# Kernel optimization log

Hardware: AMD Instinct MI355X
Metric: run time of the kernel (lower is better)

Reference implementation:

```python
import jax, jax.numpy as jnp
import numpy as np

# --- vocab metadata (replaces string itos_vocab lookups with precomputed tables) ---
# ids [0,128)   : pitch    'p0'..'p127'  (type 0)
# ids [128,289) : duration 'd0'..'d160'  (type 1)
# ids [289,390) : time     't0'..'t100'  (type 2)
# ids [390,518) : velocity 'v0'..'v127'  (type 3)
_tt = np.concatenate([np.full(128, 0), np.full(161, 1), np.full(101, 2), np.full(128, 3)]).astype(np.int32)
_tv = np.concatenate([np.arange(128), np.arange(161), np.arange(101), np.arange(128)]).astype(np.float32)
TOKEN_TYPE = jnp.asarray(_tt)   # [V]
TOKEN_VALUE = jnp.asarray(_tv)  # [V]
COEF = (1.0, 0.5, 0.5, 0.5, 0.5)  # matches init coeff_
# per-type numeric-distance normalizers (pitch unused: its branch is constant)
DENOM = jnp.array([1.0, 160.0, 100.0, 128.0], dtype=jnp.float32)
CW = jnp.array([COEF[1], COEF[2], COEF[3], COEF[4]], dtype=jnp.float32)

B, V, S = 32, 518, 2048


def setup_inputs() -> dict:
    key = jax.random.key(0)
    k1, k2 = jax.random.split(key)
    output = jax.random.normal(k1, (B, V, S), dtype=jnp.float32)  # logits [B, vocab, S]
    target = jax.random.randint(k2, (B, S), 0, V, dtype=jnp.int64)
    return {"output": output, "target": target}


def reference(output, target):
    target = target.astype(jnp.int32)
    # CrossEntropyLoss over class dim 1, mean over B*S
    lsm = jax.nn.log_softmax(output, axis=1)                       # [B,V,S]
    nll = -jnp.take_along_axis(lsm, target[:, None, :], axis=1)    # [B,1,S]
    loss = nll.mean()
    # faithful to source: softmax over last (sequence) dim, then argmax over vocab dim
    pred = jnp.argmax(jax.nn.softmax(output, axis=-1), axis=1)     # [B,S]
    pt, tt = TOKEN_TYPE[pred], TOKEN_TYPE[target]
    pv, tv = TOKEN_VALUE[pred], TOKEN_VALUE[target]
    diff = jnp.abs(pv - tv)
    # pitch branch: source compares 'pXX' != 'XX' which is always True -> constant coef[1]
    same_type = jnp.where(pt == 0, COEF[1], CW[pt] * diff / DENOM[pt])
    mask = jnp.where(pt != tt, COEF[0], same_type)                 # [B,S]
    high_cost = (loss * mask).mean()
    return loss + high_cost
```

## Files before the change

kernel.cpp:

```cpp
#include <hip/hip_runtime.h>

#define BV 518
#define SS 2048
#define NB 32

__device__ inline void tok_meta(int id, int& ty, float& val) {
    int base;
    if (id < 128)      { ty = 0; base = 0; }
    else if (id < 289) { ty = 1; base = 128; }
    else if (id < 390) { ty = 2; base = 289; }
    else               { ty = 3; base = 390; }
    val = (float)(id - base);
}

__global__ __launch_bounds__(256) void row_lse_kernel(const float* __restrict__ logits,
                                                      float* __restrict__ lse_row) {
    const int row = blockIdx.x;
    const float4* base4 = (const float4*)(logits + (size_t)row * SS);
    const int t = threadIdx.x;
    float4 x0 = base4[t];
    float4 x1 = base4[t + 256];
    float s = __expf(x0.x) + __expf(x0.y) + __expf(x0.z) + __expf(x0.w)
            + __expf(x1.x) + __expf(x1.y) + __expf(x1.z) + __expf(x1.w);
    #pragma unroll
    for (int off = 32; off; off >>= 1) s += __shfl_down(s, off);
    __shared__ float ws[4];
    if ((t & 63) == 0) ws[t >> 6] = s;
    __syncthreads();
    if (t == 0) lse_row[row] = __logf(ws[0] + ws[1] + ws[2] + ws[3]);
}

__global__ __launch_bounds__(256) void col_pass_kernel(const float* __restrict__ logits,
                                                       const int* __restrict__ target,
                                                       const float* __restrict__ lse_row,
                                                       float* __restrict__ acc) {
    const int b    = blockIdx.x >> 5;
    const int tile = blockIdx.x & 31;
    const int t    = threadIdx.x;
    const int sl   = t & 63;
    const int part = t >> 6;
    const int s    = tile * 64 + sl;

    __shared__ float slse[BV];
    for (int i = t; i < BV; i += 256) slse[i] = lse_row[b * BV + i];
    __syncthreads();

    const float* colbase = logits + (size_t)b * BV * SS + s;

    float sumexp = 0.f;
    float bscore = -1e30f;
    int   bidx   = 0x7fffffff;
    for (int v = part; v < BV; v += 4) {
        float x = colbase[(size_t)v * SS];
        sumexp += __expf(x);
        float sc = x - slse[v];
        if (sc > bscore) { bscore = sc; bidx = v; }
    }

    __shared__ float sse[4][64];
    __shared__ float sbs[4][64];
    __shared__ int   sbi[4][64];
    sse[part][sl] = sumexp;
    sbs[part][sl] = bscore;
    sbi[part][sl] = bidx;
    __syncthreads();

    if (t < 64) {
        float tot = 0.f, bs = -1e30f;
        int   bi  = 0x7fffffff;
        #pragma unroll
        for (int p = 0; p < 4; ++p) {
            tot += sse[p][t];
            float s2 = sbs[p][t]; int i2 = sbi[p][t];
            if (s2 > bs || (s2 == bs && i2 < bi)) { bs = s2; bi = i2; }
        }
        const int tgt = target[b * SS + t + tile * 64];
        const float ot = logits[(size_t)b * BV * SS + (size_t)tgt * SS + t + tile * 64];
        float nll = __logf(tot) - ot;

        int pt_, tt_; float pv_, tv_;
        tok_meta(bi, pt_, pv_);
        tok_meta(tgt, tt_, tv_);
        float mask;
        if (pt_ != tt_) {
            mask = 1.0f;
        } else if (pt_ == 0) {
            mask = 0.5f;
        } else {
            float dn = (pt_ == 1) ? 160.f : ((pt_ == 2) ? 100.f : 128.f);
            mask = 0.5f * fabsf(pv_ - tv_) / dn;
        }

        #pragma unroll
        for (int off = 32; off; off >>= 1) {
            nll  += __shfl_down(nll, off);
            mask += __shfl_down(mask, off);
        }
        if (t == 0) {
            atomicAdd(&acc[0], nll);
            atomicAdd(&acc[1], mask);
        }
    }
}

__global__ void finalize_kernel(const float* __restrict__ acc, float* __restrict__ out) {
    const float invN = 1.0f / (float)(NB * SS);
    float loss = acc[0] * invN;
    float mm   = acc[1] * invN;
    out[0] = loss * (1.0f + mm);
}

extern "C" void kernel_launch(void* const* d_in, const int* in_sizes, int n_in,
                              void* d_out, int out_size, void* d_ws, size_t ws_size,
                              hipStream_t stream) {
    const float* logits = (const float*)d_in[0];
    const int*   target = (const int*)d_in[1];
    float* outp = (float*)d_out;

    float* acc     = (float*)d_ws;
    float* lse_row = (float*)d_ws + 16;

    hipMemsetAsync(d_ws, 0, 64, stream);
    row_lse_kernel<<<NB * BV, 256, 0, stream>>>(logits, lse_row);
    col_pass_kernel<<<NB * (SS / 64), 256, 0, stream>>>(logits, target, lse_row, acc);
    finalize_kernel<<<1, 1, 0, stream>>>(acc, outp);
}
```

Measured before the change: 257.7 us.

## Split column pass over vocab halves with float4 loads and separate combine kernel

The column pass now uses float4 loads so each thread handles four sequence positions. Vocab is split into two halves across blocks, and partial sum-exp and argmax results are written to workspace. A new combine kernel merges the halves, computes the NLL and mask, and does one atomic per block instead of one per 64 columns. This aims to raise memory-level parallelism and coalescing in the column sweep, at the cost of an extra kernel launch and some partial-buffer traffic. Tie-breaking across the halves keeps the lower index only when scores are equal.

```diff
diff --git a/kernel.cpp b/kernel.cpp
--- a/kernel.cpp
+++ b/kernel.cpp
@@ -3,6 +3,7 @@
 #define BV 518
 #define SS 2048
 #define NB 32
+#define NCOL (NB * SS)
 
 __device__ inline void tok_meta(int id, int& ty, float& val) {
     int base;
@@ -30,76 +31,116 @@
     if (t == 0) lse_row[row] = __logf(ws[0] + ws[1] + ws[2] + ws[3]);
 }
 
-__global__ __launch_bounds__(256) void col_pass_kernel(const float* __restrict__ logits,
-                                                       const int* __restrict__ target,
-                                                       const float* __restrict__ lse_row,
-                                                       float* __restrict__ acc) {
-    const int b    = blockIdx.x >> 5;
-    const int tile = blockIdx.x & 31;
-    const int t    = threadIdx.x;
-    const int sl   = t & 63;
-    const int part = t >> 6;
-    const int s    = tile * 64 + sl;
+__global__ __launch_bounds__(256) void col_partial_kernel(const float* __restrict__ logits,
+                                                          const float* __restrict__ lse_row,
+                                                          float* __restrict__ pse,
+                                                          float* __restrict__ pbs,
+                                                          int*   __restrict__ pbi) {
+    const int bid   = blockIdx.x;
+    const int vh    = bid >> 8;
+    const int b     = (bid >> 3) & 31;
+    const int stile = bid & 7;
+    const int t     = threadIdx.x;
+    const int lane  = t & 63;
+    const int part  = t >> 6;
 
     __shared__ float slse[BV];
     for (int i = t; i < BV; i += 256) slse[i] = lse_row[b * BV + i];
     __syncthreads();
 
-    const float* colbase = logits + (size_t)b * BV * SS + s;
+    const int fidx = stile * 64 + lane;
+    const float4* rowbase = (const float4*)(logits + (size_t)b * BV * SS);
 
-    float sumexp = 0.f;
-    float bscore = -1e30f;
-    int   bidx   = 0x7fffffff;
-    for (int v = part; v < BV; v += 4) {
-        float x = colbase[(size_t)v * SS];
-        sumexp += __expf(x);
-        float sc = x - slse[v];
-        if (sc > bscore) { bscore = sc; bidx = v; }
+    const int vbase = vh ? 259 : 0;
+    const int vend  = vh ? BV  : 259;
+
+    float4 se = make_float4(0.f, 0.f, 0.f, 0.f);
+    float4 bs = make_float4(-1e30f, -1e30f, -1e30f, -1e30f);
+    int bix = 0x7fffffff, biy = 0x7fffffff, biz = 0x7fffffff, biw = 0x7fffffff;
+
+    #pragma unroll 4
+    for (int v = vbase + part; v < vend; v += 4) {
+        float4 x = rowbase[(size_t)v * (SS / 4) + fidx];
+        float l = slse[v];
+        se.x += __expf(x.x); se.y += __expf(x.y);
+        se.z += __expf(x.z); se.w += __expf(x.w);
+        float c0 = x.x - l, c1 = x.y - l, c2 = x.z - l, c3 = x.w - l;
+        if (c0 > bs.x) { bs.x = c0; bix = v; }
+        if (c1 > bs.y) { bs.y = c1; biy = v; }
+        if (c2 > bs.z) { bs.z = c2; biz = v; }
+        if (c3 > bs.w) { bs.w = c3; biw = v; }
     }
 
-    __shared__ float sse[4][64];
-    __shared__ float sbs[4][64];
-    __shared__ int   sbi[4][64];
-    sse[part][sl] = sumexp;
-    sbs[part][sl] = bscore;
-    sbi[part][sl] = bidx;
+    __shared__ float cse[4][256];
+    __shared__ float cbs[4][256];
+    __shared__ int   cbi[4][256];
+    const int sb = lane * 4;
+    cse[part][sb]     = se.x;  cse[part][sb + 1] = se.y;
+    cse[part][sb + 2] = se.z;  cse[part][sb + 3] = se.w;
+    cbs[part][sb]     = bs.x;  cbs[part][sb + 1] = bs.y;
+    cbs[part][sb + 2] = bs.z;  cbs[part][sb + 3] = bs.w;
+    cbi[part][sb]     = bix;   cbi[part][sb + 1] = biy;
+    cbi[part][sb + 2] = biz;   cbi[part][sb + 3] = biw;
     __syncthreads();
 
-    if (t < 64) {
-        float tot = 0.f, bs = -1e30f;
-        int   bi  = 0x7fffffff;
-        #pragma unroll
-        for (int p = 0; p < 4; ++p) {
-            tot += sse[p][t];
-            float s2 = sbs[p][t]; int i2 = sbi[p][t];
-            if (s2 > bs || (s2 == bs && i2 < bi)) { bs = s2; bi = i2; }
-        }
-        const int tgt = target[b * SS + t + tile * 64];
-        const float ot = logits[(size_t)b * BV * SS + (size_t)tgt * SS + t + tile * 64];
-        float nll = __logf(tot) - ot;
+    float tot = 0.f, best = -1e30f;
+    int   bi  = 0x7fffffff;
+    #pragma unroll
+    for (int p = 0; p < 4; ++p) {
+        tot += cse[p][t];
+        float s2 = cbs[p][t]; int i2 = cbi[p][t];
+        if (s2 > best || (s2 == best && i2 < bi)) { best = s2; bi = i2; }
+    }
+    const int g = (b * 8 + stile) * 256 + t;
+    pse[vh * NCOL + g] = tot;
+    pbs[vh * NCOL + g] = best;
+    pbi[vh * NCOL + g] = bi;
+}
 
-        int pt_, tt_; float pv_, tv_;
-        tok_meta(bi, pt_, pv_);
-        tok_meta(tgt, tt_, tv_);
-        float mask;
-        if (pt_ != tt_) {
-            mask = 1.0f;
-        } else if (pt_ == 0) {
-            mask = 0.5f;
-        } else {
-            float dn = (pt_ == 1) ? 160.f : ((pt_ == 2) ? 100.f : 128.f);
-            mask = 0.5f * fabsf(pv_ - tv_) / dn;
-        }
+__global__ __launch_bounds__(256) void combine_kernel(const float* __restrict__ logits,
+                                                      const int* __restrict__ target,
+                                                      const float* __restrict__ pse,
+                                                      const float* __restrict__ pbs,
+                                                      const int* __restrict__ pbi,
+                                                      float* __restrict__ acc) {
+    const int t = threadIdx.x;
+    const int g = blockIdx.x * 256 + t;
+    const int b = g >> 11;
+    const int s = g & 2047;
 
-        #pragma unroll
-        for (int off = 32; off; off >>= 1) {
-            nll  += __shfl_down(nll, off);
-            mask += __shfl_down(mask, off);
-        }
-        if (t == 0) {
-            atomicAdd(&acc[0], nll);
-            atomicAdd(&acc[1], mask);
-        }
+    float tot = pse[g] + pse[NCOL + g];
+    float b0 = pbs[g];        int i0 = pbi[g];
+    float b1 = pbs[NCOL + g]; int i1 = pbi[NCOL + g];
+    int bi = (b1 > b0) ? i1 : i0;
+
+    const int tgt = target[g];
+    const float ot = logits[(size_t)(b * BV + tgt) * SS + s];
+    float nll = __logf(tot) - ot;
+
+    int pt_, tt_; float pv_, tv_;
+    tok_meta(bi, pt_, pv_);
+    tok_meta(tgt, tt_, tv_);
+    float mask;
+    if (pt_ != tt_) {
+        mask = 1.0f;
+    } else if (pt_ == 0) {
+        mask = 0.5f;
+    } else {
+        float dn = (pt_ == 1) ? 160.f : ((pt_ == 2) ? 100.f : 128.f);
+        mask = 0.5f * fabsf(pv_ - tv_) / dn;
+    }
+
+    #pragma unroll
+    for (int off = 32; off; off >>= 1) {
+        nll  += __shfl_down(nll, off);
+        mask += __shfl_down(mask, off);
+    }
+    __shared__ float wn[4], wm[4];
+    if ((t & 63) == 0) { wn[t >> 6] = nll; wm[t >> 6] = mask; }
+    __syncthreads();
+    if (t == 0) {
+        atomicAdd(&acc[0], wn[0] + wn[1] + wn[2] + wn[3]);
+        atomicAdd(&acc[1], wm[0] + wm[1] + wm[2] + wm[3]);
     }
 }
 
@@ -118,10 +159,14 @@
     float* outp = (float*)d_out;
 
     float* acc     = (float*)d_ws;
-    float* lse_row = (float*)d_ws + 16;
+    float* lse_row = (float*)d_ws + 64;
+    float* pse     = (float*)d_ws + 17024;
+    float* pbs     = pse + 2 * NCOL;
+    int*   pbi     = (int*)(pbs + 2 * NCOL);
 
     hipMemsetAsync(d_ws, 0, 64, stream);
     row_lse_kernel<<<NB * BV, 256, 0, stream>>>(logits, lse_row);
-    col_pass_kernel<<<NB * (SS / 64), 256, 0, stream>>>(logits, target, lse_row, acc);
+    col_partial_kernel<<<512, 256, 0, stream>>>(logits, lse_row, pse, pbs, pbi);
+    combine_kernel<<<NCOL / 256, 256, 0, stream>>>(logits, target, pse, pbs, pbi, acc);
     finalize_kernel<<<1, 1, 0, stream>>>(acc, outp);
 }
```

Result: faster. 223.5 us (-13.3%).

## Fuse row LSE and column pass into one chunked kernel with atomic merge

Applied to the files above, without the earlier changes.

Replaces the separate row log-sum-exp pass and the full-column pass with one kernel. Each block handles a 16-row vocab chunk for one batch. It computes each row's LSE, then rereads those rows (likely from cache) to update per-column sumexp and argmax. Partial results go to global arrays through float atomicAdd and a packed 64-bit atomicMax, so the logits are effectively streamed from HBM once instead of twice. The cost is a large workspace memset, many global atomics, and an extra combine kernel.

```diff
diff --git a/kernel.cpp b/kernel.cpp
--- a/kernel.cpp
+++ b/kernel.cpp
@@ -3,6 +3,9 @@
 #define BV 518
 #define SS 2048
 #define NB 32
+#define NCOL (NB * SS)
+#define CHUNK 16
+#define NCH 33
 
 __device__ inline void tok_meta(int id, int& ty, float& val) {
     int base;
@@ -13,101 +16,135 @@
     val = (float)(id - base);
 }
 
-__global__ __launch_bounds__(256) void row_lse_kernel(const float* __restrict__ logits,
-                                                      float* __restrict__ lse_row) {
-    const int row = blockIdx.x;
-    const float4* base4 = (const float4*)(logits + (size_t)row * SS);
+__global__ __launch_bounds__(256, 2) void colfused_kernel(const float* __restrict__ logits,
+                                                          float* __restrict__ sacc,
+                                                          unsigned long long* __restrict__ pmax) {
+    const int bid = blockIdx.x;
+    const int b   = bid / NCH;
+    const int c   = bid % NCH;
+    const int v0  = c * CHUNK;
+    const int nrows = (BV - v0 < CHUNK) ? (BV - v0) : CHUNK;
     const int t = threadIdx.x;
-    float4 x0 = base4[t];
-    float4 x1 = base4[t + 256];
-    float s = __expf(x0.x) + __expf(x0.y) + __expf(x0.z) + __expf(x0.w)
-            + __expf(x1.x) + __expf(x1.y) + __expf(x1.z) + __expf(x1.w);
+    const int w = t >> 6;
+    const int l = t & 63;
+
+    __shared__ float slse[2][4];
+    const float* base = logits + (size_t)(b * BV) * SS;
+
+    float se[8];  float bsc[8];  int bvi[8];
     #pragma unroll
-    for (int off = 32; off; off >>= 1) s += __shfl_down(s, off);
-    __shared__ float ws[4];
-    if ((t & 63) == 0) ws[t >> 6] = s;
-    __syncthreads();
-    if (t == 0) lse_row[row] = __logf(ws[0] + ws[1] + ws[2] + ws[3]);
-}
+    for (int u = 0; u < 8; ++u) { se[u] = 0.f; bsc[u] = -1e30f; bvi[u] = 0; }
 
-__global__ __launch_bounds__(256) void col_pass_kernel(const float* __restrict__ logits,
-                                                       const int* __restrict__ target,
-                                                       const float* __restrict__ lse_row,
-                                                       float* __restrict__ acc) {
-    const int b    = blockIdx.x >> 5;
-    const int tile = blockIdx.x & 31;
-    const int t    = threadIdx.x;
-    const int sl   = t & 63;
-    const int part = t >> 6;
-    const int s    = tile * 64 + sl;
+    const int nsub = (nrows + 3) >> 2;
+    for (int sub = 0; sub < nsub; ++sub) {
+        const int r0 = sub * 4;
+        const int myrow = r0 + w;
+        if (myrow < nrows) {
+            const float4* rb = (const float4*)(base + (size_t)(v0 + myrow) * SS);
+            float s = 0.f;
+            #pragma unroll
+            for (int j = 0; j < 8; ++j) {
+                float4 x = rb[l + 64 * j];
+                s += __expf(x.x) + __expf(x.y) + __expf(x.z) + __expf(x.w);
+            }
+            #pragma unroll
+            for (int off = 32; off; off >>= 1) s += __shfl_xor(s, off);
+            if (l == 0) slse[sub & 1][w] = __logf(s);
+        }
+        __syncthreads();
 
-    __shared__ float slse[BV];
-    for (int i = t; i < BV; i += 256) slse[i] = lse_row[b * BV + i];
-    __syncthreads();
-
-    const float* colbase = logits + (size_t)b * BV * SS + s;
-
-    float sumexp = 0.f;
-    float bscore = -1e30f;
-    int   bidx   = 0x7fffffff;
-    for (int v = part; v < BV; v += 4) {
-        float x = colbase[(size_t)v * SS];
-        sumexp += __expf(x);
-        float sc = x - slse[v];
-        if (sc > bscore) { bscore = sc; bidx = v; }
+        const int rend = (nrows - r0 < 4) ? (nrows - r0) : 4;
+        for (int r = 0; r < rend; ++r) {
+            const int v = v0 + r0 + r;
+            const float lse = slse[sub & 1][r];
+            const float* rowp = base + (size_t)v * SS;
+            #pragma unroll
+            for (int u = 0; u < 8; ++u) {
+                float x = rowp[u * 256 + t];
+                se[u] += __expf(x);
+                float sc = x - lse;
+                if (sc > bsc[u]) { bsc[u] = sc; bvi[u] = v; }
+            }
+        }
     }
 
-    __shared__ float sse[4][64];
-    __shared__ float sbs[4][64];
-    __shared__ int   sbi[4][64];
-    sse[part][sl] = sumexp;
-    sbs[part][sl] = bscore;
-    sbi[part][sl] = bidx;
-    __syncthreads();
-
-    if (t < 64) {
-        float tot = 0.f, bs = -1e30f;
-        int   bi  = 0x7fffffff;
-        #pragma unroll
-        for (int p = 0; p < 4; ++p) {
-            tot += sse[p][t];
-            float s2 = sbs[p][t]; int i2 = sbi[p][t];
-            if (s2 > bs || (s2 == bs && i2 < bi)) { bs = s2; bi = i2; }
-        }
-        const int tgt = target[b * SS + t + tile * 64];
-        const float ot = logits[(size_t)b * BV * SS + (size_t)tgt * SS + t + tile * 64];
-        float nll = __logf(tot) - ot;
-
-        int pt_, tt_; float pv_, tv_;
-        tok_meta(bi, pt_, pv_);
-        tok_meta(tgt, tt_, tv_);
-        float mask;
-        if (pt_ != tt_) {
-            mask = 1.0f;
-        } else if (pt_ == 0) {
-            mask = 0.5f;
-        } else {
-            float dn = (pt_ == 1) ? 160.f : ((pt_ == 2) ? 100.f : 128.f);
-            mask = 0.5f * fabsf(pv_ - tv_) / dn;
-        }
-
-        #pragma unroll
-        for (int off = 32; off; off >>= 1) {
-            nll  += __shfl_down(nll, off);
-            mask += __shfl_down(mask, off);
-        }
-        if (t == 0) {
-            atomicAdd(&acc[0], nll);
-            atomicAdd(&acc[1], mask);
-        }
+    #pragma unroll
+    for (int u = 0; u < 8; ++u) {
+        const int g = b * SS + u * 256 + t;
+        atomicAdd(&sacc[g], se[u]);
+        unsigned int ub = __float_as_uint(bsc[u]);
+        ub = (ub & 0x80000000u) ? ~ub : (ub | 0x80000000u);
+        unsigned long long packed = ((unsigned long long)ub << 32)
+                                  | (unsigned long long)(0xFFFFu - (unsigned)bvi[u]);
+        atomicMax(&pmax[g], packed);
     }
 }
 
-__global__ void finalize_kernel(const float* __restrict__ acc, float* __restrict__ out) {
-    const float invN = 1.0f / (float)(NB * SS);
-    float loss = acc[0] * invN;
-    float mm   = acc[1] * invN;
-    out[0] = loss * (1.0f + mm);
+__global__ __launch_bounds__(256) void combine_kernel(const float* __restrict__ logits,
+                                                      const int* __restrict__ target,
+                                                      const float* __restrict__ sacc,
+                                                      const unsigned long long* __restrict__ pmax,
+                                                      float* __restrict__ pnll,
+                                                      float* __restrict__ pmask) {
+    const int t = threadIdx.x;
+    const int g = blockIdx.x * 256 + t;
+    const int b = g >> 11;
+    const int s = g & 2047;
+
+    const float tot = sacc[g];
+    const unsigned long long p = pmax[g];
+    const int bi  = 0xFFFF - (int)(p & 0xFFFFull);
+    const int tgt = target[g];
+    const float ot = logits[(size_t)(b * BV + tgt) * SS + s];
+    float nll = __logf(tot) - ot;
+
+    int pt_, tt_; float pv_, tv_;
+    tok_meta(bi, pt_, pv_);
+    tok_meta(tgt, tt_, tv_);
+    float mask;
+    if (pt_ != tt_) {
+        mask = 1.0f;
+    } else if (pt_ == 0) {
+        mask = 0.5f;
+    } else {
+        float dn = (pt_ == 1) ? 160.f : ((pt_ == 2) ? 100.f : 128.f);
+        mask = 0.5f * fabsf(pv_ - tv_) / dn;
+    }
+
+    #pragma unroll
+    for (int off = 32; off; off >>= 1) {
+        nll  += __shfl_down(nll, off);
+        mask += __shfl_down(mask, off);
+    }
+    __shared__ float wn[4], wm[4];
+    if ((t & 63) == 0) { wn[t >> 6] = nll; wm[t >> 6] = mask; }
+    __syncthreads();
+    if (t == 0) {
+        pnll[blockIdx.x]  = wn[0] + wn[1] + wn[2] + wn[3];
+        pmask[blockIdx.x] = wm[0] + wm[1] + wm[2] + wm[3];
+    }
+}
+
+__global__ __launch_bounds__(256) void finalize_kernel(const float* __restrict__ pnll,
+                                                       const float* __restrict__ pmask,
+                                                       float* __restrict__ out) {
+    const int t = threadIdx.x;
+    float n = pnll[t];
+    float m = pmask[t];
+    #pragma unroll
+    for (int off = 32; off; off >>= 1) {
+        n += __shfl_down(n, off);
+        m += __shfl_down(m, off);
+    }
+    __shared__ float wn[4], wm[4];
+    if ((t & 63) == 0) { wn[t >> 6] = n; wm[t >> 6] = m; }
+    __syncthreads();
+    if (t == 0) {
+        const float invN = 1.0f / (float)NCOL;
+        float loss = (wn[0] + wn[1] + wn[2] + wn[3]) * invN;
+        float mm   = (wm[0] + wm[1] + wm[2] + wm[3]) * invN;
+        out[0] = loss * (1.0f + mm);
+    }
 }
 
 extern "C" void kernel_launch(void* const* d_in, const int* in_sizes, int n_in,
@@ -117,11 +154,13 @@
     const int*   target = (const int*)d_in[1];
     float* outp = (float*)d_out;
 
-    float* acc     = (float*)d_ws;
-    float* lse_row = (float*)d_ws + 16;
+    float*              sacc  = (float*)d_ws;
+    unsigned long long* pmax  = (unsigned long long*)((char*)d_ws + (NCOL * 4));
+    float*              pnll  = (float*)((char*)d_ws + (NCOL * 12));
+    float*              pmask = pnll + 256;
 
-    hipMemsetAsync(d_ws, 0, 64, stream);
-    row_lse_kernel<<<NB * BV, 256, 0, stream>>>(logits, lse_row);
-    col_pass_kernel<<<NB * (SS / 64), 256, 0, stream>>>(logits, target, lse_row, acc);
-    finalize_kernel<<<1, 1, 0, stream>>>(acc, outp);
+    hipMemsetAsync(d_ws, 0, NCOL * 12, stream);
+    colfused_kernel<<<NB * NCH, 256, 0, stream>>>(logits, sacc, pmax);
+    combine_kernel<<<NCOL / 256, 256, 0, stream>>>(logits, target, sacc, pmax, pnll, pmask);
+    finalize_kernel<<<1, 256, 0, stream>>>(pnll, pmask, outp);
 }
```

Result: faster. 212.3 us (-17.6%).
